# Kernel optimization log

Hardware: AMD Instinct MI355X
Metric: run time of the kernel (lower is better)

The kernel has to match this reference:

```python
import jax, jax.numpy as jnp
import numpy as np

TEMP = 0.07
BASE_TEMP = 0.07
EPS = 1e-12


def setup_inputs() -> dict:
    key = jax.random.key(0)
    k1, k2, k3 = jax.random.split(key, 3)
    B, V, D, C = 4096, 1, 128, 100
    features = jax.random.normal(k1, (B, V, D), dtype=jnp.float32)
    labels = jax.random.randint(k2, (B,), 0, C, dtype=jnp.int64)
    covariances = jax.random.normal(k3, (C, D, D), dtype=jnp.float32)
    return {"features": features, "labels": labels, "covariances": covariances}


def reference(features, labels, covariances):
    B, n_views = features.shape[0], features.shape[1]
    feats = features.reshape(B, n_views, -1)
    # cat(unbind(dim=1), dim=0); with n_views==1 this is feats[:, 0]
    contrast_feature = jnp.concatenate([feats[:, v] for v in range(n_views)], axis=0)
    anchor_feature = contrast_feature  # contrast_mode == 'all'

    # mask_{i,j} = 1 if labels match
    mask = (labels[:, None] == labels[None, :]).astype(jnp.float32)  # [B,B]

    similarity_matrix = anchor_feature @ contrast_feature.T  # [B,B]

    # dis[i,j] = a_i^T C_{label_i} a_j  (gather cov per anchor, one bilinear form per pair)
    cov_g = covariances[labels]                              # [B,D,D] irregular gather
    v = jnp.einsum('id,ide->ie', anchor_feature, cov_g)      # [B,D]
    dis_matrix = v @ anchor_feature.T                        # [B,B]

    logits = (similarity_matrix + dis_matrix / (2.0 * TEMP ** 2)) / TEMP
    logits = logits - jax.lax.stop_gradient(jnp.max(logits, axis=1, keepdims=True))
    log_prob = logits - jnp.log(jnp.sum(jnp.exp(logits), axis=1, keepdims=True) + EPS)

    # original: (mask[:,:,None] * log_prob).sum(1) == mask @ log_prob (avoids B^3 temp)
    mask_sum = mask.sum(axis=1, keepdims=True)               # [B,1]
    mean_log_prob_pos = (mask @ log_prob) / (mask_sum + EPS)  # [B,B]
    loss = -(TEMP / BASE_TEMP) * mean_log_prob_pos
    return loss.mean()
```

## Files before the change

### kernel.cpp

```cpp
#include <hip/hip_runtime.h>
#include <hip/hip_bf16.h>


#define DIM 128
#define TEMP 0.07f
#define PITCH 136

typedef __attribute__((ext_vector_type(8))) short short8;
typedef __attribute__((ext_vector_type(4))) float floatx4;

static __device__ __forceinline__ unsigned short f2bf(float f) {
    __hip_bfloat16 h = __float2bfloat16(f);
    union { __hip_bfloat16 h; unsigned short u; } c;
    c.h = h;
    return c.u;
}

__global__ __launch_bounds__(256) void prep_kernel(
    const float* __restrict__ A, const int* __restrict__ labels,
    const float* __restrict__ Cov, unsigned short* __restrict__ Wbf,
    unsigned short* __restrict__ Abf, double* __restrict__ G,
    int* __restrict__ counts, int C) {
    const float inv2t2 = 1.0f / (2.0f * TEMP * TEMP);
    const float invt = 1.0f / TEMP;
    const int sub = threadIdx.x >> 7;
    const int e = threadIdx.x & 127;
    const int i = blockIdx.x * 2 + sub;
    __shared__ float a[2][DIM];
    float av = A[(size_t)i * DIM + e];
    a[sub][e] = av;
    Abf[(size_t)i * DIM + e] = f2bf(av);
    if (blockIdx.x == 0) {
        int t = threadIdx.x;
        if (t < C) { G[t] = 0.0; counts[t] = 0; }
    }
    __syncthreads();
    int c = labels[i];
    const float* Cp = Cov + (size_t)c * (DIM * DIM) + e;
    float acc = 0.0f;
#pragma unroll 8
    for (int d = 0; d < DIM; ++d) {
        acc = fmaf(a[sub][d], Cp[(size_t)d * DIM], acc);
    }
    Wbf[(size_t)i * DIM + e] = f2bf((av + acc * inv2t2) * invt);
}

__global__ __launch_bounds__(256, 2) void main_kernel(
    const unsigned short* __restrict__ Wbf, const unsigned short* __restrict__ Abf,
    float* __restrict__ mP, float* __restrict__ zP, float* __restrict__ sP,
    int Jsplit, int JSWEEP, int nP) {
    __shared__ __align__(16) unsigned short sW[128 * PITCH];
    __shared__ __align__(16) unsigned short sA[64 * PITCH];

    const int mb = blockIdx.x / Jsplit;
    const int jsp = blockIdx.x % Jsplit;
    const int rowBase = mb * 128;
    const int t = threadIdx.x;
    const int wave = t >> 6, lane = t & 63, quad = lane >> 4, l16 = lane & 15;
    const int waveM = wave >> 1, waveN = wave & 1;

    {
        int row = t >> 1, half = t & 1;
        const unsigned short* src = Wbf + (size_t)(rowBase + row) * DIM + half * 64;
        unsigned short* dst = sW + row * PITCH + half * 64;
#pragma unroll
        for (int i = 0; i < 8; i++)
            *(short8*)(dst + i * 8) = *(const short8*)(src + i * 8);
    }

    float run_m[4][4], run_Z[4][4], run_s[4][4];
#pragma unroll
    for (int a = 0; a < 4; a++)
#pragma unroll
        for (int r = 0; r < 4; r++) {
            run_m[a][r] = -3.4e38f; run_Z[a][r] = 0.f; run_s[a][r] = 0.f;
        }

    const unsigned short* myW = sW + (waveM * 64 + l16) * PITCH;
    const unsigned short* myA = sA + (waveN * 32 + l16) * PITCH;

    for (int js = 0; js < JSWEEP; ++js) {
        __syncthreads();
        {
            int row = t >> 2, q = t & 3;
            int j0 = (jsp * JSWEEP + js) * 64;
            const unsigned short* src = Abf + (size_t)(j0 + row) * DIM + q * 32;
            unsigned short* dst = sA + row * PITCH + q * 32;
#pragma unroll
            for (int i = 0; i < 4; i++)
                *(short8*)(dst + i * 8) = *(const short8*)(src + i * 8);
        }
        __syncthreads();

        floatx4 acc[4][2];
#pragma unroll
        for (int mt = 0; mt < 4; mt++)
#pragma unroll
            for (int nt = 0; nt < 2; nt++) acc[mt][nt] = (floatx4)0.f;

#pragma unroll
        for (int kst = 0; kst < 4; ++kst) {
            const int koff = kst * 32 + quad * 8;
            short8 bfrag[2];
#pragma unroll
            for (int nt = 0; nt < 2; nt++)
                bfrag[nt] = *(const short8*)(myA + nt * 16 * PITCH + koff);
#pragma unroll
            for (int mt = 0; mt < 4; mt++) {
                short8 afrag = *(const short8*)(myW + mt * 16 * PITCH + koff);
#pragma unroll
                for (int nt = 0; nt < 2; nt++)
                    acc[mt][nt] = __builtin_amdgcn_mfma_f32_16x16x32_bf16(
                        afrag, bfrag[nt], acc[mt][nt], 0, 0, 0);
            }
        }

#pragma unroll
        for (int mt = 0; mt < 4; mt++)
#pragma unroll
            for (int r = 0; r < 4; r++) {
                float v0 = acc[mt][0][r], v1 = acc[mt][1][r];
                float tm = fmaxf(v0, v1);
                float nm = fmaxf(run_m[mt][r], tm);
                run_Z[mt][r] = run_Z[mt][r] * __expf(run_m[mt][r] - nm)
                             + __expf(v0 - nm) + __expf(v1 - nm);
                run_m[mt][r] = nm;
                run_s[mt][r] += v0 + v1;
            }
    }

    const int chunk = jsp * 2 + waveN;
#pragma unroll
    for (int mt = 0; mt < 4; mt++)
#pragma unroll
        for (int r = 0; r < 4; r++) {
            float m = run_m[mt][r], Z = run_Z[mt][r], s = run_s[mt][r];
#pragma unroll
            for (int mask = 1; mask < 16; mask <<= 1) {
                float om = __shfl_xor(m, mask);
                float oZ = __shfl_xor(Z, mask);
                float os = __shfl_xor(s, mask);
                float nm = fmaxf(m, om);
                Z = Z * __expf(m - nm) + oZ * __expf(om - nm);
                m = nm;
                s += os;
            }
            if (l16 == r) {
                int row = rowBase + waveM * 64 + mt * 16 + quad * 4 + r;
                size_t idx = (size_t)row * nP + chunk;
                mP[idx] = m; zP[idx] = Z; sP[idx] = s;
            }
        }
}

__global__ __launch_bounds__(64) void combine_kernel(
    const float* __restrict__ mP, const float* __restrict__ zP,
    const float* __restrict__ sP, const int* __restrict__ labels,
    double* __restrict__ G, int* __restrict__ counts, int B, int nP) {
    int k = blockIdx.x;
    int l = threadIdx.x;
    float m = -3.4e38f, Z = 0.0f, s = 0.0f;
    if (l < nP) {
        size_t idx = (size_t)k * nP + l;
        m = mP[idx]; Z = zP[idx]; s = sP[idx];
    }
    float M = m;
#pragma unroll
    for (int o = 32; o > 0; o >>= 1) M = fmaxf(M, __shfl_xor(M, o));
    float zt = Z * __expf(m - M);
    float st = s;
#pragma unroll
    for (int o = 32; o > 0; o >>= 1) {
        zt += __shfl_xor(zt, o);
        st += __shfl_xor(st, o);
    }
    if (l == 0) {
        double Sk = (double)st - (double)B * (double)M
                    - (double)B * log((double)zt + 1e-12);
        int c = labels[k];
        atomicAdd(&G[c], Sk);
        atomicAdd(&counts[c], 1);
    }
}

__global__ __launch_bounds__(128) void final_kernel(
    const double* __restrict__ G, const int* __restrict__ counts,
    float* __restrict__ out, int C, double invB2) {
    __shared__ double sh[128];
    int t = threadIdx.x;
    double v = 0.0;
    if (t < C) {
        double cnt = (double)counts[t];
        v = G[t] * (cnt / (cnt + 1e-12));
    }
    sh[t] = v;
    __syncthreads();
    for (int o = 64; o > 0; o >>= 1) {
        if (t < o) sh[t] += sh[t + o];
        __syncthreads();
    }
    if (t == 0) out[0] = (float)(-sh[0] * invB2);
}

extern "C" void kernel_launch(void* const* d_in, const int* in_sizes, int n_in,
                              void* d_out, int out_size, void* d_ws, size_t ws_size,
                              hipStream_t stream) {
    const float* A = (const float*)d_in[0];
    const int* labels = (const int*)d_in[1];
    const float* Cov = (const float*)d_in[2];
    float* out = (float*)d_out;

    int B = in_sizes[0] / DIM;
    int C = in_sizes[2] / (DIM * DIM);
    int Jsplit = 16;
    int JSWEEP = B / (Jsplit * 64);
    int nP = Jsplit * 2;

    char* ws = (char*)d_ws;
    unsigned short* Wbf = (unsigned short*)ws;
    unsigned short* Abf = Wbf + (size_t)B * DIM;
    float* mP = (float*)(Abf + (size_t)B * DIM);
    float* zP = mP + (size_t)B * nP;
    float* sP = zP + (size_t)B * nP;
    double* G = (double*)(sP + (size_t)B * nP);
    int* counts = (int*)(G + C);

    prep_kernel<<<B / 2, 256, 0, stream>>>(A, labels, Cov, Wbf, Abf,
                                           G, counts, C);
    main_kernel<<<(B / 128) * Jsplit, 256, 0, stream>>>(Wbf, Abf, mP, zP, sP,
                                                        Jsplit, JSWEEP, nP);
    combine_kernel<<<B, 64, 0, stream>>>(mP, zP, sP, labels, G, counts, B, nP);
    final_kernel<<<1, 128, 0, stream>>>(G, counts, out, C,
                                        1.0 / ((double)B * (double)B));
}
```

Before: 109.4 us.

## Group rows by class so each covariance matrix is read once per tile

Adds a single-block counting sort that buckets anchor rows by label. A per-class kernel then computes a_i^T C_c for up to 32 rows at a time as a register-blocked outer product, reusing each covariance load instead of gathering the full 64KB matrix once per row. Per-class counts now come from the sort, so the combine kernel drops its count atomic. The cost is one extra serial single-block launch, plus load imbalance because each class has about 41 rows spread over only 100 blocks.

```diff
diff --git a/kernel.cpp b/kernel.cpp
--- a/kernel.cpp
+++ b/kernel.cpp
@@ -5,6 +5,7 @@
 #define DIM 128
 #define TEMP 0.07f
 #define PITCH 136
+#define RT 32
 
 typedef __attribute__((ext_vector_type(8))) short short8;
 typedef __attribute__((ext_vector_type(4))) float floatx4;
@@ -16,33 +17,122 @@
     return c.u;
 }
 
-__global__ __launch_bounds__(256) void prep_kernel(
-    const float* __restrict__ A, const int* __restrict__ labels,
-    const float* __restrict__ Cov, unsigned short* __restrict__ Wbf,
-    unsigned short* __restrict__ Abf, double* __restrict__ G,
-    int* __restrict__ counts, int C) {
+__global__ __launch_bounds__(1024) void sort_kernel(
+    const int* __restrict__ labels, int* __restrict__ order,
+    int* __restrict__ classStart, int* __restrict__ counts,
+    double* __restrict__ G, int B, int C) {
+    __shared__ int hist[128];
+    __shared__ int offs[132];
+    int t = threadIdx.x;
+    if (t < 128) hist[t] = 0;
+    __syncthreads();
+    for (int i = t; i < B; i += 1024) atomicAdd(&hist[labels[i]], 1);
+    __syncthreads();
+    if (t == 0) {
+        int s = 0;
+        for (int c = 0; c < C; ++c) { offs[c] = s; s += hist[c]; }
+        offs[C] = s;
+    }
+    __syncthreads();
+    if (t < C) {
+        counts[t] = hist[t];
+        G[t] = 0.0;
+        classStart[t] = offs[t];
+    }
+    if (t == C) classStart[C] = offs[C];
+    __syncthreads();
+    if (t < C) hist[t] = offs[t];
+    __syncthreads();
+    for (int i = t; i < B; i += 1024) {
+        int pos = atomicAdd(&hist[labels[i]], 1);
+        order[pos] = i;
+    }
+}
+
+__global__ __launch_bounds__(256) void wbuild_kernel(
+    const float* __restrict__ A, const float* __restrict__ Cov,
+    const int* __restrict__ order, const int* __restrict__ classStart,
+    unsigned short* __restrict__ Wbf, unsigned short* __restrict__ Abf) {
     const float inv2t2 = 1.0f / (2.0f * TEMP * TEMP);
     const float invt = 1.0f / TEMP;
-    const int sub = threadIdx.x >> 7;
-    const int e = threadIdx.x & 127;
-    const int i = blockIdx.x * 2 + sub;
-    __shared__ float a[2][DIM];
-    float av = A[(size_t)i * DIM + e];
-    a[sub][e] = av;
-    Abf[(size_t)i * DIM + e] = f2bf(av);
-    if (blockIdx.x == 0) {
-        int t = threadIdx.x;
-        if (t < C) { G[t] = 0.0; counts[t] = 0; }
-    }
-    __syncthreads();
-    int c = labels[i];
-    const float* Cp = Cov + (size_t)c * (DIM * DIM) + e;
-    float acc = 0.0f;
+    const int c = blockIdx.x;
+    const int start = classStart[c], end = classStart[c + 1];
+    const int t = threadIdx.x;
+    __shared__ float aT[DIM][RT];
+    const float* CovC = Cov + (size_t)c * DIM * DIM;
+
+    for (int r0 = start; r0 < end; r0 += RT) {
+        int nr = end - r0;
+        if (nr > RT) nr = RT;
+        __syncthreads();
+        {
+            int rl = t & 31, dseg = (t >> 5) * 16;
+            if (rl < nr) {
+                int row = order[r0 + rl];
+                const float4* src = (const float4*)(A + (size_t)row * DIM + dseg);
+                float4 v[4];
+#pragma unroll
+                for (int i = 0; i < 4; ++i) v[i] = src[i];
+                ushort4* ad = (ushort4*)(Abf + (size_t)row * DIM + dseg);
+#pragma unroll
+                for (int i = 0; i < 4; ++i) {
+                    ushort4 o;
+                    o.x = f2bf(v[i].x); o.y = f2bf(v[i].y);
+                    o.z = f2bf(v[i].z); o.w = f2bf(v[i].w);
+                    ad[i] = o;
+                }
+#pragma unroll
+                for (int i = 0; i < 4; ++i) {
+                    aT[dseg + i * 4 + 0][rl] = v[i].x;
+                    aT[dseg + i * 4 + 1][rl] = v[i].y;
+                    aT[dseg + i * 4 + 2][rl] = v[i].z;
+                    aT[dseg + i * 4 + 3][rl] = v[i].w;
+                }
+            }
+        }
+        __syncthreads();
+        const int rg = t >> 5, e0 = (t & 31) * 4;
+        float4 acc[4];
+#pragma unroll
+        for (int i = 0; i < 4; ++i) acc[i] = make_float4(0.f, 0.f, 0.f, 0.f);
+        const float* cp = CovC + e0;
 #pragma unroll 8
-    for (int d = 0; d < DIM; ++d) {
-        acc = fmaf(a[sub][d], Cp[(size_t)d * DIM], acc);
-    }
-    Wbf[(size_t)i * DIM + e] = f2bf((av + acc * inv2t2) * invt);
+        for (int d = 0; d < DIM; ++d) {
+            float4 cv = *(const float4*)(cp + (size_t)d * DIM);
+            float4 av = *(const float4*)&aT[d][rg * 4];
+            acc[0].x = fmaf(cv.x, av.x, acc[0].x);
+            acc[0].y = fmaf(cv.y, av.x, acc[0].y);
+            acc[0].z = fmaf(cv.z, av.x, acc[0].z);
+            acc[0].w = fmaf(cv.w, av.x, acc[0].w);
+            acc[1].x = fmaf(cv.x, av.y, acc[1].x);
+            acc[1].y = fmaf(cv.y, av.y, acc[1].y);
+            acc[1].z = fmaf(cv.z, av.y, acc[1].z);
+            acc[1].w = fmaf(cv.w, av.y, acc[1].w);
+            acc[2].x = fmaf(cv.x, av.z, acc[2].x);
+            acc[2].y = fmaf(cv.y, av.z, acc[2].y);
+            acc[2].z = fmaf(cv.z, av.z, acc[2].z);
+            acc[2].w = fmaf(cv.w, av.z, acc[2].w);
+            acc[3].x = fmaf(cv.x, av.w, acc[3].x);
+            acc[3].y = fmaf(cv.y, av.w, acc[3].y);
+            acc[3].z = fmaf(cv.z, av.w, acc[3].z);
+            acc[3].w = fmaf(cv.w, av.w, acc[3].w);
+        }
+#pragma unroll
+        for (int rr = 0; rr < 4; ++rr) {
+            int rl2 = rg * 4 + rr;
+            if (rl2 < nr) {
+                int row = order[r0 + rl2];
+                float ax = aT[e0 + 0][rl2], ay = aT[e0 + 1][rl2];
+                float az = aT[e0 + 2][rl2], aw = aT[e0 + 3][rl2];
+                ushort4 w;
+                w.x = f2bf((ax + acc[rr].x * inv2t2) * invt);
+                w.y = f2bf((ay + acc[rr].y * inv2t2) * invt);
+                w.z = f2bf((az + acc[rr].z * inv2t2) * invt);
+                w.w = f2bf((aw + acc[rr].w * inv2t2) * invt);
+                *(ushort4*)(Wbf + (size_t)row * DIM + e0) = w;
+            }
+        }
+    }
 }
 
 __global__ __launch_bounds__(256, 2) void main_kernel(
@@ -156,7 +246,7 @@
 __global__ __launch_bounds__(64) void combine_kernel(
     const float* __restrict__ mP, const float* __restrict__ zP,
     const float* __restrict__ sP, const int* __restrict__ labels,
-    double* __restrict__ G, int* __restrict__ counts, int B, int nP) {
+    double* __restrict__ G, int B, int nP) {
     int k = blockIdx.x;
     int l = threadIdx.x;
     float m = -3.4e38f, Z = 0.0f, s = 0.0f;
@@ -177,9 +267,7 @@
     if (l == 0) {
         double Sk = (double)st - (double)B * (double)M
                     - (double)B * log((double)zt + 1e-12);
-        int c = labels[k];
-        atomicAdd(&G[c], Sk);
-        atomicAdd(&counts[c], 1);
+        atomicAdd(&G[labels[k]], Sk);
     }
 }
 
@@ -224,12 +312,15 @@
     float* sP = zP + (size_t)B * nP;
     double* G = (double*)(sP + (size_t)B * nP);
     int* counts = (int*)(G + C);
-
-    prep_kernel<<<B / 2, 256, 0, stream>>>(A, labels, Cov, Wbf, Abf,
-                                           G, counts, C);
+    int* order = counts + C;
+    int* classStart = order + B;
+
+    sort_kernel<<<1, 1024, 0, stream>>>(labels, order, classStart, counts,
+                                        G, B, C);
+    wbuild_kernel<<<C, 256, 0, stream>>>(A, Cov, order, classStart, Wbf, Abf);
     main_kernel<<<(B / 128) * Jsplit, 256, 0, stream>>>(Wbf, Abf, mP, zP, sP,
                                                         Jsplit, JSWEEP, nP);
-    combine_kernel<<<B, 64, 0, stream>>>(mP, zP, sP, labels, G, counts, B, nP);
+    combine_kernel<<<B, 64, 0, stream>>>(mP, zP, sP, labels, G, B, nP);
     final_kernel<<<1, 128, 0, stream>>>(G, counts, out, C,
                                         1.0 / ((double)B * (double)B));
 }
```

Result: slower. 113.1 us (+3.3%).

## Swizzle LDS tiles, prefetch next A tile into registers, drop global atomics

Applied to the files above, without the earlier changes.

Replaces the padded LDS pitch with an XOR-swizzled 128-wide layout, which cuts shared memory use and avoids bank conflicts. The next contrast tile is now loaded into registers while the current tile's MFMAs run, overlapping global loads with compute. The per-class double atomics in combine are removed. Each row's score is stored instead, and a single 1024-thread final block builds a label histogram and reduces the scores. This makes the final kernel serial over B and adds register pressure from the prefetch buffer.

```diff
diff --git a/kernel.cpp b/kernel.cpp
--- a/kernel.cpp
+++ b/kernel.cpp
@@ -4,7 +4,6 @@
 
 #define DIM 128
 #define TEMP 0.07f
-#define PITCH 136
 
 typedef __attribute__((ext_vector_type(8))) short short8;
 typedef __attribute__((ext_vector_type(4))) float floatx4;
@@ -19,8 +18,7 @@
 __global__ __launch_bounds__(256) void prep_kernel(
     const float* __restrict__ A, const int* __restrict__ labels,
     const float* __restrict__ Cov, unsigned short* __restrict__ Wbf,
-    unsigned short* __restrict__ Abf, double* __restrict__ G,
-    int* __restrict__ counts, int C) {
+    unsigned short* __restrict__ Abf) {
     const float inv2t2 = 1.0f / (2.0f * TEMP * TEMP);
     const float invt = 1.0f / TEMP;
     const int sub = threadIdx.x >> 7;
@@ -30,10 +28,6 @@
     float av = A[(size_t)i * DIM + e];
     a[sub][e] = av;
     Abf[(size_t)i * DIM + e] = f2bf(av);
-    if (blockIdx.x == 0) {
-        int t = threadIdx.x;
-        if (t < C) { G[t] = 0.0; counts[t] = 0; }
-    }
     __syncthreads();
     int c = labels[i];
     const float* Cp = Cov + (size_t)c * (DIM * DIM) + e;
@@ -49,8 +43,8 @@
     const unsigned short* __restrict__ Wbf, const unsigned short* __restrict__ Abf,
     float* __restrict__ mP, float* __restrict__ zP, float* __restrict__ sP,
     int Jsplit, int JSWEEP, int nP) {
-    __shared__ __align__(16) unsigned short sW[128 * PITCH];
-    __shared__ __align__(16) unsigned short sA[64 * PITCH];
+    __shared__ __align__(16) unsigned short sW[128 * 128];
+    __shared__ __align__(16) unsigned short sA[64 * 128];
 
     const int mb = blockIdx.x / Jsplit;
     const int jsp = blockIdx.x % Jsplit;
@@ -60,12 +54,14 @@
     const int waveM = wave >> 1, waveN = wave & 1;
 
     {
-        int row = t >> 1, half = t & 1;
+        int row = t >> 1, half = t & 1, rsw = row & 15;
         const unsigned short* src = Wbf + (size_t)(rowBase + row) * DIM + half * 64;
-        unsigned short* dst = sW + row * PITCH + half * 64;
-#pragma unroll
-        for (int i = 0; i < 8; i++)
-            *(short8*)(dst + i * 8) = *(const short8*)(src + i * 8);
+        unsigned short* dstrow = sW + row * 128;
+#pragma unroll
+        for (int i = 0; i < 8; i++) {
+            int c = half * 8 + i;
+            *(short8*)(dstrow + ((c ^ rsw) << 3)) = *(const short8*)(src + i * 8);
+        }
     }
 
     float run_m[4][4], run_Z[4][4], run_s[4][4];
@@ -76,22 +72,33 @@
             run_m[a][r] = -3.4e38f; run_Z[a][r] = 0.f; run_s[a][r] = 0.f;
         }
 
-    const unsigned short* myW = sW + (waveM * 64 + l16) * PITCH;
-    const unsigned short* myA = sA + (waveN * 32 + l16) * PITCH;
+    const int arow = t >> 2, aq = t & 3, arsw = arow & 15;
+    const unsigned short* asrc0 =
+        Abf + (size_t)(jsp * JSWEEP * 64 + arow) * DIM + aq * 32;
+    unsigned short* adst = sA + arow * 128;
+
+    short8 pre[4];
+#pragma unroll
+    for (int i = 0; i < 4; i++) pre[i] = *(const short8*)(asrc0 + i * 8);
+
+    const unsigned short* myW = sW + (size_t)(waveM * 64 + l16) * 128;
+    const unsigned short* myA = sA + (size_t)(waveN * 32 + l16) * 128;
 
     for (int js = 0; js < JSWEEP; ++js) {
         __syncthreads();
-        {
-            int row = t >> 2, q = t & 3;
-            int j0 = (jsp * JSWEEP + js) * 64;
-            const unsigned short* src = Abf + (size_t)(j0 + row) * DIM + q * 32;
-            unsigned short* dst = sA + row * PITCH + q * 32;
-#pragma unroll
-            for (int i = 0; i < 4; i++)
-                *(short8*)(dst + i * 8) = *(const short8*)(src + i * 8);
+#pragma unroll
+        for (int i = 0; i < 4; i++) {
+            int c = aq * 4 + i;
+            *(short8*)(adst + ((c ^ arsw) << 3)) = pre[i];
         }
         __syncthreads();
 
+        if (js + 1 < JSWEEP) {
+            const unsigned short* nsrc = asrc0 + (size_t)(js + 1) * 64 * DIM;
+#pragma unroll
+            for (int i = 0; i < 4; i++) pre[i] = *(const short8*)(nsrc + i * 8);
+        }
+
         floatx4 acc[4][2];
 #pragma unroll
         for (int mt = 0; mt < 4; mt++)
@@ -100,14 +107,14 @@
 
 #pragma unroll
         for (int kst = 0; kst < 4; ++kst) {
-            const int koff = kst * 32 + quad * 8;
+            const int coff = (((kst << 2) | quad) ^ l16) << 3;
             short8 bfrag[2];
 #pragma unroll
             for (int nt = 0; nt < 2; nt++)
-                bfrag[nt] = *(const short8*)(myA + nt * 16 * PITCH + koff);
+                bfrag[nt] = *(const short8*)(myA + nt * 16 * 128 + coff);
 #pragma unroll
             for (int mt = 0; mt < 4; mt++) {
-                short8 afrag = *(const short8*)(myW + mt * 16 * PITCH + koff);
+                short8 afrag = *(const short8*)(myW + mt * 16 * 128 + coff);
 #pragma unroll
                 for (int nt = 0; nt < 2; nt++)
                     acc[mt][nt] = __builtin_amdgcn_mfma_f32_16x16x32_bf16(
@@ -155,8 +162,7 @@
 
 __global__ __launch_bounds__(64) void combine_kernel(
     const float* __restrict__ mP, const float* __restrict__ zP,
-    const float* __restrict__ sP, const int* __restrict__ labels,
-    double* __restrict__ G, int* __restrict__ counts, int B, int nP) {
+    const float* __restrict__ sP, double* __restrict__ Sk, int B, int nP) {
     int k = blockIdx.x;
     int l = threadIdx.x;
     float m = -3.4e38f, Z = 0.0f, s = 0.0f;
@@ -175,31 +181,33 @@
         st += __shfl_xor(st, o);
     }
     if (l == 0) {
-        double Sk = (double)st - (double)B * (double)M
-                    - (double)B * log((double)zt + 1e-12);
-        int c = labels[k];
-        atomicAdd(&G[c], Sk);
-        atomicAdd(&counts[c], 1);
-    }
-}
-
-__global__ __launch_bounds__(128) void final_kernel(
-    const double* __restrict__ G, const int* __restrict__ counts,
-    float* __restrict__ out, int C, double invB2) {
-    __shared__ double sh[128];
+        Sk[k] = (double)st - (double)B * (double)M
+                - (double)B * log((double)zt + 1e-12);
+    }
+}
+
+__global__ __launch_bounds__(1024) void final_kernel(
+    const double* __restrict__ Sk, const int* __restrict__ labels,
+    float* __restrict__ out, int B) {
+    __shared__ int hist[128];
+    __shared__ double sh[1024];
     int t = threadIdx.x;
-    double v = 0.0;
-    if (t < C) {
-        double cnt = (double)counts[t];
-        v = G[t] * (cnt / (cnt + 1e-12));
-    }
-    sh[t] = v;
-    __syncthreads();
-    for (int o = 64; o > 0; o >>= 1) {
+    if (t < 128) hist[t] = 0;
+    __syncthreads();
+    for (int i = t; i < B; i += 1024) atomicAdd(&hist[labels[i]], 1);
+    __syncthreads();
+    double acc = 0.0;
+    for (int i = t; i < B; i += 1024) {
+        double cnt = (double)hist[labels[i]];
+        acc += Sk[i] * (cnt / (cnt + 1e-12));
+    }
+    sh[t] = acc;
+    __syncthreads();
+    for (int o = 512; o > 0; o >>= 1) {
         if (t < o) sh[t] += sh[t + o];
         __syncthreads();
     }
-    if (t == 0) out[0] = (float)(-sh[0] * invB2);
+    if (t == 0) out[0] = (float)(-sh[0] / ((double)B * (double)B));
 }
 
 extern "C" void kernel_launch(void* const* d_in, const int* in_sizes, int n_in,
@@ -211,7 +219,6 @@
     float* out = (float*)d_out;
 
     int B = in_sizes[0] / DIM;
-    int C = in_sizes[2] / (DIM * DIM);
     int Jsplit = 16;
     int JSWEEP = B / (Jsplit * 64);
     int nP = Jsplit * 2;
@@ -222,14 +229,11 @@
     float* mP = (float*)(Abf + (size_t)B * DIM);
     float* zP = mP + (size_t)B * nP;
     float* sP = zP + (size_t)B * nP;
-    double* G = (double*)(sP + (size_t)B * nP);
-    int* counts = (int*)(G + C);
-
-    prep_kernel<<<B / 2, 256, 0, stream>>>(A, labels, Cov, Wbf, Abf,
-                                           G, counts, C);
+    double* Sk = (double*)(sP + (size_t)B * nP);
+
+    prep_kernel<<<B / 2, 256, 0, stream>>>(A, labels, Cov, Wbf, Abf);
     main_kernel<<<(B / 128) * Jsplit, 256, 0, stream>>>(Wbf, Abf, mP, zP, sP,
                                                         Jsplit, JSWEEP, nP);
-    combine_kernel<<<B, 64, 0, stream>>>(mP, zP, sP, labels, G, counts, B, nP);
-    final_kernel<<<1, 128, 0, stream>>>(G, counts, out, C,
-                                        1.0 / ((double)B * (double)B));
-}
+    combine_kernel<<<B, 64, 0, stream>>>(mP, zP, sP, Sk, B, nP);
+    final_kernel<<<1, 1024, 0, stream>>>(Sk, labels, out, B);
+}
```

New measurement: 101.0 us (median of 2 runs). 1.08x faster.
